# Kernel optimization log

Measured on AMD Instinct MI355X. Metric: run time of the kernel, lower is better.

## Reference

```python
import jax, jax.numpy as jnp
import numpy as np

EPS_BN = 1e-5
EPS_LN = 1e-5
EPS_L2 = 1e-12


def adder2d(x, w, stride):
    """AdderNet pseudo-conv: out = -sum |x_patch - w| (negative L1 distance).
    x: (N, Cin, H, W); w: (Cout, Cin, kh, kw); no padding, no bias.
    Loops only over the small fixed kernel footprint (<=12 positions) to avoid
    materializing the full im2col L1 tensor at once.
    """
    N, Cin, H, W = x.shape
    Cout, _, kh, kw = w.shape
    sh, sw = stride
    Ho = (H - kh) // sh + 1
    Wo = (W - kw) // sw + 1
    out = jnp.zeros((N, Ho, Wo, Cout), dtype=x.dtype)
    for i in range(kh):
        for j in range(kw):
            # strided slice of the input for this kernel tap: (N, Cin, Ho, Wo)
            xs = x[:, :, i:i + sh * Ho:sh, j:j + sw * Wo:sw]
            xs = jnp.transpose(xs, (0, 2, 3, 1))          # (N, Ho, Wo, Cin)
            wt = w[:, :, i, j]                            # (Cout, Cin)
            # |x - w| summed over Cin -> (N, Ho, Wo, Cout)
            out = out - jnp.abs(xs[:, :, :, None, :] - wt[None, None, None, :, :]).sum(-1)
    return jnp.transpose(out, (0, 3, 1, 2))               # (N, Cout, Ho, Wo)


def bn_relu(x, gamma, beta):
    # training-mode BatchNorm2d (batch statistics, biased var) + ReLU
    mean = x.mean(axis=(0, 2, 3), keepdims=True)
    var = x.var(axis=(0, 2, 3), keepdims=True)
    y = (x - mean) * jax.lax.rsqrt(var + EPS_BN)
    y = y * gamma[None, :, None, None] + beta[None, :, None, None]
    return jax.nn.relu(y)


def setup_inputs() -> dict:
    key = jax.random.key(0)
    ks = jax.random.split(key, 8)
    N = 16
    x = jax.random.normal(ks[0], (N, 1, 196, 3), dtype=jnp.float32)
    w1 = jax.random.normal(ks[1], (128, 1, 6, 1), dtype=jnp.float32) * 0.1
    w2 = jax.random.normal(ks[2], (256, 128, 6, 1), dtype=jnp.float32) * 0.05
    w3 = jax.random.normal(ks[3], (384, 256, 6, 2), dtype=jnp.float32) * 0.05
    g1, b1 = jnp.ones((128,), jnp.float32), jnp.zeros((128,), jnp.float32)
    g2, b2 = jnp.ones((256,), jnp.float32), jnp.zeros((256,), jnp.float32)
    g3, b3 = jnp.ones((384,), jnp.float32), jnp.zeros((384,), jnp.float32)
    Wfc = jax.random.normal(ks[4], (6, 16128), dtype=jnp.float32) * (1.0 / np.sqrt(16128))
    bfc = jax.random.normal(ks[5], (6,), dtype=jnp.float32) * 0.01
    return {"x": x, "w1": w1, "g1": g1, "b1": b1, "w2": w2, "g2": g2, "b2": b2,
            "w3": w3, "g3": g3, "b3": b3, "Wfc": Wfc, "bfc": bfc}


def reference(x, w1, g1, b1, w2, g2, b2, w3, g3, b3, Wfc, bfc):
    h = bn_relu(adder2d(x, w1, (2, 1)), g1, b1)   # (N,128,96,3)
    h = bn_relu(adder2d(h, w2, (2, 1)), g2, b2)   # (N,256,46,3)
    h = bn_relu(adder2d(h, w3, (2, 1)), g3, b3)   # (N,384,21,2)
    h = h.reshape(h.shape[0], -1)                  # (N,16128)
    h = h @ Wfc.T + bfc                            # (N,6)
    # nn.LayerNorm(x.size()) normalizes over ALL dims (batch included), weight=1 bias=0
    mu = h.mean()
    var = h.var()
    h = (h - mu) * jax.lax.rsqrt(var + EPS_LN)
    # F.normalize: per-row L2 normalization
    norm = jnp.sqrt((h * h).sum(axis=1, keepdims=True))
    return h / jnp.maximum(norm, EPS_L2)
```

## Files before the change

### kernel.cpp

```cpp
#include <hip/hip_runtime.h>
#include <math.h>

#define DEVINL __device__ __forceinline__

DEVINL float absadd(float a, float b) {
  float t;
  asm("v_add_f32 %0, |%1|, |%2|" : "=v"(t) : "v"(a), "v"(b));
  return t;
}

template<int NWAVES>
DEVINL void block_reduce_2d(double& a, double& b) {
  #pragma unroll
  for (int off = 32; off > 0; off >>= 1) {
    a += __shfl_down(a, off, 64);
    b += __shfl_down(b, off, 64);
  }
  __shared__ double sa[NWAVES], sb[NWAVES];
  const int tid = threadIdx.x;
  const int wid = tid >> 6;
  if ((tid & 63) == 0) { sa[wid] = a; sb[wid] = b; }
  __syncthreads();
  if (tid == 0) {
    double ta = 0.0, tb = 0.0;
    #pragma unroll
    for (int w = 0; w < NWAVES; ++w) { ta += sa[w]; tb += sb[w]; }
    a = ta; b = tb;
  }
}

__global__ __launch_bounds__(256) void k_conv1(
    const float* __restrict__ x, const float* __restrict__ w1,
    const float* __restrict__ g1, const float* __restrict__ b1,
    float* __restrict__ h1) {
  __shared__ float xlds[9408];
  const int co = blockIdx.x;
  const int tid = threadIdx.x;
  {
    float4* xd = (float4*)xlds;
    const float4* xs = (const float4*)x;
    #pragma unroll
    for (int k = 0; k < 10; ++k) {
      const int f = tid + k * 256;
      if (f < 2352) xd[f] = xs[f];
    }
  }
  float wv[6];
  #pragma unroll
  for (int i = 0; i < 6; ++i) wv[i] = w1[co * 6 + i];
  __syncthreads();

  float vals[18];
  double s = 0.0, sq = 0.0;
  #pragma unroll
  for (int k = 0; k < 18; ++k) {
    const int p = tid + k * 256;
    const int n = p / 288;
    const int r = p - n * 288;
    const int ho = r / 3;
    const int wo = r - ho * 3;
    const float* xb = xlds + n * 588 + (2 * ho) * 3 + wo;
    float e0 = xb[0]  - wv[0];
    float e1 = xb[3]  - wv[1];
    float e2 = xb[6]  - wv[2];
    float e3 = xb[9]  - wv[3];
    float e4 = xb[12] - wv[4];
    float e5 = xb[15] - wv[5];
    const float t0 = absadd(e0, e1);
    const float t1 = absadd(e2, e3);
    const float t2 = absadd(e4, e5);
    const float v = -((t0 + t1) + t2);
    vals[k] = v;
    s += (double)v;
    sq += (double)v * (double)v;
  }
  block_reduce_2d<4>(s, sq);
  __shared__ float ssc, ssh;
  if (tid == 0) {
    const double mean = s * (1.0 / 4608.0);
    const double var  = sq * (1.0 / 4608.0) - mean * mean;
    const float rstd = (float)rsqrt(var + 1e-5);
    const float sc = g1[co] * rstd;
    ssc = sc;
    ssh = b1[co] - (float)mean * sc;
  }
  __syncthreads();
  const float sc = ssc, sh = ssh;
  #pragma unroll
  for (int k = 0; k < 18; ++k) {
    const int p = tid + k * 256;
    const int n = p / 288;
    const int r = p - n * 288;
    const int ho = r / 3;
    const int wo = r - ho * 3;
    h1[((n * 128 + co) * 96 + ho) * 3 + wo] = fmaxf(0.f, fmaf(vals[k], sc, sh));
  }
}

__global__ __launch_bounds__(128) void k_conv2p(
    const float* __restrict__ h1, const float* __restrict__ w2,
    float* __restrict__ part2) {
  __shared__ float wlds[1024];
  __shared__ float2 xbuf[2][616];
  __shared__ float accbuf[64][71];
  const int bx = blockIdx.x;
  const int kc = bx & 7;
  const int rbx = bx >> 3;
  const int cg = rbx & 31;
  const int rbx2 = rbx >> 5;
  const int hoh = rbx2 & 1;
  const int nh = rbx2 >> 1;
  const int co0 = cg * 8, ci0 = kc * 16, n0 = nh * 8;
  const int tid = threadIdx.x;
  const int wvid = tid >> 6;
  const int lane = tid & 63;
  #pragma unroll
  for (int k = 0; k < 8; ++k) {
    const int f = wvid * 512 + lane + k * 64;
    const int cil = f >> 6, rem = f & 63, c = rem >> 3, kk = rem & 7;
    wlds[f] = (kk < 6) ? w2[(co0 + c) * 768 + (ci0 + cil) * 6 + kk] : 0.f;
  }
  const int n = lane >> 3, co = lane & 7;

  int s_lds[10], s_g[10];
  const bool v10 = lane < 24;
  #pragma unroll
  for (int k = 0; k < 10; ++k) {
    const int f = lane + k * 64;
    const int nn = f / 75, j = f - nn * 75;
    s_lds[k] = nn * 77 + j;
    s_g[k]   = (n0 + nn) * 18432 + 69 * hoh + j;
  }
  const float2* h1v = (const float2*)h1;
  const int cibase = ci0 + wvid * 8;

  float acc[69];
  #pragma unroll
  for (int i = 0; i < 69; ++i) acc[i] = 0.f;

  float2 r[10];
  #pragma unroll
  for (int k = 0; k < 9; ++k) r[k] = h1v[s_g[k] + cibase * 144];
  if (v10) r[9] = h1v[s_g[9] + cibase * 144];

  const float2* xrow2 = xbuf[wvid] + n * 77;
  const float4* wl4 = (const float4*)wlds;

  #pragma unroll 1
  for (int cil = 0; cil < 8; ++cil) {
    #pragma unroll
    for (int k = 0; k < 9; ++k) xbuf[wvid][s_lds[k]] = r[k];
    if (v10) xbuf[wvid][s_lds[9]] = r[9];
    if (cil + 1 < 8) {
      #pragma unroll
      for (int k = 0; k < 9; ++k) r[k] = h1v[s_g[k] + (cibase + cil + 1) * 144];
      if (v10) r[9] = h1v[s_g[9] + (cibase + cil + 1) * 144];
    }
    const int cl = wvid * 8 + cil;
    const float4 wa = wl4[(cl * 8 + co) * 2];
    const float4 wb = wl4[(cl * 8 + co) * 2 + 1];
    const float wv[6] = {wa.x, wa.y, wa.z, wa.w, wb.x, wb.y};
    float xf[18];
    #pragma unroll
    for (int t = 0; t < 9; ++t) {
      const float2 q = xrow2[t];
      xf[2 * t] = q.x; xf[2 * t + 1] = q.y;
    }
    #pragma unroll
    for (int h = 0; h < 23; ++h) {
      if (h > 0) {
        #pragma unroll
        for (int t = 0; t < 12; ++t) xf[t] = xf[t + 6];
        #pragma unroll
        for (int t = 0; t < 3; ++t) {
          const float2 q = xrow2[3 * h + 6 + t];
          xf[12 + 2 * t] = q.x; xf[13 + 2 * t] = q.y;
        }
      }
      #pragma unroll
      for (int wo = 0; wo < 3; ++wo) {
        float e0 = xf[0  + wo] - wv[0];
        float e1 = xf[3  + wo] - wv[1];
        float e2 = xf[6  + wo] - wv[2];
        float e3 = xf[9  + wo] - wv[3];
        float e4 = xf[12 + wo] - wv[4];
        float e5 = xf[15 + wo] - wv[5];
        const float t0 = absadd(e0, e1);
        const float t1 = absadd(e2, e3);
        const float t2 = absadd(e4, e5);
        acc[h * 3 + wo] += (t0 + t1) + t2;
      }
    }
  }
  if (wvid == 1) {
    #pragma unroll
    for (int i = 0; i < 69; ++i) accbuf[lane][i] = acc[i];
  }
  __syncthreads();
  if (wvid == 0) {
    #pragma unroll
    for (int i = 0; i < 69; ++i) acc[i] += accbuf[lane][i];
    float* dst = part2 + (size_t)(kc * 256 + co0 + co) * 2208 + (n0 + n) * 138 + 69 * hoh;
    #pragma unroll
    for (int i = 0; i < 69; ++i) dst[i] = acc[i];
  }
}

__global__ __launch_bounds__(384) void k_combine2(
    const float* __restrict__ part2, const float* __restrict__ g2,
    const float* __restrict__ b2, float* __restrict__ h2) {
  const int co = blockIdx.x;
  const int tid = threadIdx.x;
  const bool active = tid < 368;
  float v[6];
  double s = 0.0, sq = 0.0;
  #pragma unroll
  for (int k = 0; k < 6; ++k) {
    float sum = 0.f;
    if (active) {
      const int p = tid + k * 368;
      #pragma unroll
      for (int kc = 0; kc < 8; ++kc)
        sum += part2[(size_t)(kc * 256 + co) * 2208 + p];
    }
    const float val = -sum;
    v[k] = val;
    if (active) { s += (double)val; sq += (double)val * (double)val; }
  }
  block_reduce_2d<6>(s, sq);
  __shared__ float ssc, ssh;
  if (tid == 0) {
    const double mean = s * (1.0 / 2208.0);
    const double var  = sq * (1.0 / 2208.0) - mean * mean;
    const float rstd = (float)rsqrt(var + 1e-5);
    const float sc = g2[co] * rstd;
    ssc = sc;
    ssh = b2[co] - (float)mean * sc;
  }
  __syncthreads();
  if (active) {
    const float sc = ssc, sh = ssh;
    #pragma unroll
    for (int k = 0; k < 6; ++k) {
      const int p = tid + k * 368;
      const int n = p / 138, rem = p - n * 138;
      h2[n * 35328 + co * 138 + rem] = fmaxf(0.f, fmaf(v[k], sc, sh));
    }
  }
}

__global__ __launch_bounds__(128) void k_conv3p(
    const float* __restrict__ h2, const float* __restrict__ w3,
    float* __restrict__ part3) {
  __shared__ float wlds[1536];
  __shared__ float2 xbuf[2][560];
  __shared__ float accbuf[64][43];
  const int bx = blockIdx.x;
  const int kc = bx & 15;
  const int rbx = bx >> 4;
  const int cg = rbx % 48;
  const int nh = rbx / 48;
  const int co0 = cg * 8, ci0 = kc * 16, n0 = nh * 8;
  const int tid = threadIdx.x;
  const int wvid = tid >> 6;
  const int lane = tid & 63;
  #pragma unroll
  for (int k = 0; k < 12; ++k) {
    const int f = wvid * 768 + lane + k * 64;
    const int cil = f / 96, rem = f - cil * 96, c = rem / 12, kk = rem - c * 12;
    wlds[f] = w3[(co0 + c) * 3072 + (ci0 + cil) * 12 + kk];
  }
  const int n = lane >> 3, co = lane & 7;

  int s_lds[9], s_g[9];
  const bool v9 = lane < 40;
  #pragma unroll
  for (int k = 0; k < 9; ++k) {
    const int f = lane + k * 64;
    const int nn = f / 69, j = f - nn * 69;
    s_lds[k] = nn * 70 + j;
    s_g[k]   = (n0 + nn) * 17664 + j;
  }
  const float2* h2v = (const float2*)h2;
  const int cibase = ci0 + wvid * 8;

  float acc[42];
  #pragma unroll
  for (int i = 0; i < 42; ++i) acc[i] = 0.f;

  float2 r[9];
  #pragma unroll
  for (int k = 0; k < 8; ++k) r[k] = h2v[s_g[k] + cibase * 69];
  if (v9) r[8] = h2v[s_g[8] + cibase * 69];

  const float2* xrow2 = xbuf[wvid] + n * 70;
  const float4* wl4 = (const float4*)wlds;

  #pragma unroll 1
  for (int cil = 0; cil < 8; ++cil) {
    #pragma unroll
    for (int k = 0; k < 8; ++k) xbuf[wvid][s_lds[k]] = r[k];
    if (v9) xbuf[wvid][s_lds[8]] = r[8];
    if (cil + 1 < 8) {
      #pragma unroll
      for (int k = 0; k < 8; ++k) r[k] = h2v[s_g[k] + (cibase + cil + 1) * 69];
      if (v9) r[8] = h2v[s_g[8] + (cibase + cil + 1) * 69];
    }
    const int cl = wvid * 8 + cil;
    const float4 w0 = wl4[(cl * 8 + co) * 3];
    const float4 w1 = wl4[(cl * 8 + co) * 3 + 1];
    const float4 w2q = wl4[(cl * 8 + co) * 3 + 2];
    const float wv[12] = {w0.x, w0.y, w0.z, w0.w, w1.x, w1.y,
                          w1.z, w1.w, w2q.x, w2q.y, w2q.z, w2q.w};
    float xf[30];
    #pragma unroll
    for (int t = 0; t < 15; ++t) {
      const float2 q = xrow2[t];
      xf[2 * t + 0] = q.x; xf[2 * t + 1] = q.y;
    }
    #pragma unroll
    for (int hot = 0; hot < 7; ++hot) {
      #pragma unroll
      for (int h = 0; h < 3; ++h)
        #pragma unroll
        for (int wo = 0; wo < 2; ++wo) {
          float e0  = xf[(2 * h + 0) * 3 + wo]     - wv[0];
          float e1  = xf[(2 * h + 0) * 3 + wo + 1] - wv[1];
          float e2  = xf[(2 * h + 1) * 3 + wo]     - wv[2];
          float e3  = xf[(2 * h + 1) * 3 + wo + 1] - wv[3];
          float e4  = xf[(2 * h + 2) * 3 + wo]     - wv[4];
          float e5  = xf[(2 * h + 2) * 3 + wo + 1] - wv[5];
          float e6  = xf[(2 * h + 3) * 3 + wo]     - wv[6];
          float e7  = xf[(2 * h + 3) * 3 + wo + 1] - wv[7];
          float e8  = xf[(2 * h + 4) * 3 + wo]     - wv[8];
          float e9  = xf[(2 * h + 4) * 3 + wo + 1] - wv[9];
          float e10 = xf[(2 * h + 5) * 3 + wo]     - wv[10];
          float e11 = xf[(2 * h + 5) * 3 + wo + 1] - wv[11];
          const float t0 = absadd(e0, e1);
          const float t1 = absadd(e2, e3);
          const float t2 = absadd(e4, e5);
          const float t3 = absadd(e6, e7);
          const float t4 = absadd(e8, e9);
          const float t5 = absadd(e10, e11);
          acc[(3 * hot + h) * 2 + wo] += ((t0 + t1) + (t2 + t3)) + (t4 + t5);
        }
      if (hot < 6) {
        #pragma unroll
        for (int t = 0; t < 12; ++t) xf[t] = xf[t + 18];
        #pragma unroll
        for (int t = 0; t < 9; ++t) {
          const float2 q = xrow2[9 * hot + 15 + t];
          xf[12 + 2 * t] = q.x; xf[13 + 2 * t] = q.y;
        }
      }
    }
  }
  if (wvid == 1) {
    #pragma unroll
    for (int i = 0; i < 42; ++i) accbuf[lane][i] = acc[i];
  }
  __syncthreads();
  if (wvid == 0) {
    #pragma unroll
    for (int i = 0; i < 42; ++i) acc[i] += accbuf[lane][i];
    float2* dst = (float2*)(part3 + (size_t)(kc * 384 + co0 + co) * 672 + (n0 + n) * 42);
    #pragma unroll
    for (int k = 0; k < 21; ++k) dst[k] = make_float2(acc[2 * k], acc[2 * k + 1]);
  }
}

__global__ __launch_bounds__(384) void k_combine3(
    const float* __restrict__ part3, const float* __restrict__ g3,
    const float* __restrict__ b3, float* __restrict__ h3) {
  const int co = blockIdx.x;
  const int tid = threadIdx.x;
  const bool active = tid < 336;
  float v[2];
  double s = 0.0, sq = 0.0;
  #pragma unroll
  for (int k = 0; k < 2; ++k) {
    float sum = 0.f;
    if (active) {
      const int p = tid + k * 336;
      #pragma unroll
      for (int kc = 0; kc < 16; ++kc)
        sum += part3[(size_t)(kc * 384 + co) * 672 + p];
    }
    const float val = -sum;
    v[k] = val;
    if (active) { s += (double)val; sq += (double)val * (double)val; }
  }
  block_reduce_2d<6>(s, sq);
  __shared__ float ssc, ssh;
  if (tid == 0) {
    const double mean = s * (1.0 / 672.0);
    const double var  = sq * (1.0 / 672.0) - mean * mean;
    const float rstd = (float)rsqrt(var + 1e-5);
    const float sc = g3[co] * rstd;
    ssc = sc;
    ssh = b3[co] - (float)mean * sc;
  }
  __syncthreads();
  if (active) {
    const float sc = ssc, sh = ssh;
    #pragma unroll
    for (int k = 0; k < 2; ++k) {
      const int p = tid + k * 336;
      const int n = p / 42, rem = p - n * 42;
      h3[n * 16128 + co * 42 + rem] = fmaxf(0.f, fmaf(v[k], sc, sh));
    }
  }
}

__global__ __launch_bounds__(256) void k_fcp(
    const float* __restrict__ h3, const float* __restrict__ Wfc,
    float* __restrict__ hfcp) {
  const int bx = blockIdx.x;
  const int pair = bx >> 2, q = bx & 3;
  const int n = pair / 6, o = pair - n * 6;
  const float4* xr = (const float4*)(h3 + n * 16128) + q * 1008;
  const float4* wr = (const float4*)(Wfc + o * 16128) + q * 1008;
  float sacc = 0.f;
  for (int k = threadIdx.x; k < 1008; k += 256) {
    const float4 xv = xr[k];
    const float4 wv = wr[k];
    sacc += xv.x * wv.x + xv.y * wv.y + xv.z * wv.z + xv.w * wv.w;
  }
  double d = (double)sacc, dummy = 0.0;
  block_reduce_2d<4>(d, dummy);
  if (threadIdx.x == 0) hfcp[bx] = (float)d;
}

__global__ __launch_bounds__(128) void k_final(
    const float* __restrict__ hfcp, const float* __restrict__ bfc,
    float* __restrict__ out) {
  __shared__ float ys[96];
  __shared__ float params[2];
  const int tid = threadIdx.x;
  float v = 0.f;
  if (tid < 96) {
    v = hfcp[tid * 4 + 0] + hfcp[tid * 4 + 1] + hfcp[tid * 4 + 2] + hfcp[tid * 4 + 3]
        + bfc[tid % 6];
    ys[tid] = v;
  }
  __syncthreads();
  if (tid == 0) {
    double s = 0.0, sq = 0.0;
    for (int i = 0; i < 96; ++i) { const double t = (double)ys[i]; s += t; sq += t * t; }
    const double mu = s / 96.0;
    const double var = sq / 96.0 - mu * mu;
    params[0] = (float)mu;
    params[1] = (float)rsqrt(var + 1e-5);
  }
  __syncthreads();
  const float y = (v - params[0]) * params[1];
  __syncthreads();
  if (tid < 96) ys[tid] = y;
  __syncthreads();
  if (tid < 96) {
    const int n = tid / 6;
    float ss = 0.f;
    #pragma unroll
    for (int k = 0; k < 6; ++k) { const float t = ys[n * 6 + k]; ss += t * t; }
    const float norm = sqrtf(ss);
    out[tid] = y / fmaxf(norm, 1e-12f);
  }
}

extern "C" void kernel_launch(void* const* d_in, const int* in_sizes, int n_in,
                              void* d_out, int out_size, void* d_ws, size_t ws_size,
                              hipStream_t stream) {
  const float* x   = (const float*)d_in[0];
  const float* w1  = (const float*)d_in[1];
  const float* g1  = (const float*)d_in[2];
  const float* b1  = (const float*)d_in[3];
  const float* w2  = (const float*)d_in[4];
  const float* g2  = (const float*)d_in[5];
  const float* b2  = (const float*)d_in[6];
  const float* w3  = (const float*)d_in[7];
  const float* g3  = (const float*)d_in[8];
  const float* b3  = (const float*)d_in[9];
  const float* Wfc = (const float*)d_in[10];
  const float* bfc = (const float*)d_in[11];

  float* ws   = (float*)d_ws;
  float* h1   = ws;
  float* h2   = h1 + 589824;
  float* h3   = h2 + 565248;
  float* hfcp = h3 + 258048;
  float* part = hfcp + 384;
  float* out  = (float*)d_out;

  k_conv1   <<<128, 256, 0, stream>>>(x, w1, g1, b1, h1);
  k_conv2p  <<<1024, 128, 0, stream>>>(h1, w2, part);
  k_combine2<<<256, 384, 0, stream>>>(part, g2, b2, h2);
  k_conv3p  <<<1536, 128, 0, stream>>>(h2, w3, part);
  k_combine3<<<384, 384, 0, stream>>>(part, g3, b3, h3);
  k_fcp     <<<384, 256, 0, stream>>>(h3, Wfc, hfcp);
  k_final   <<<1, 128, 0, stream>>>(hfcp, bfc, out);
}
```

Baseline: 108.9 us.

## Split input-channel chunk across four waves per block in conv2/conv3 partial kernels

The two adder-conv partial kernels now launch 256 threads (four waves) per block instead of 128. Each wave handles 4 input channels instead of 8, which halves the serial per-wave loop and doubles the waves available to hide latency. The cross-wave reduction is rewritten as a chunked LDS reduction that reuses the input staging buffer. The cost is extra shared-memory reduction passes and barriers, plus more register pressure per block, which could limit occupancy given the large per-thread accumulator arrays.

```diff
diff --git a/kernel.cpp b/kernel.cpp
--- a/kernel.cpp
+++ b/kernel.cpp
@@ -97,12 +97,11 @@
   }
 }
 
-__global__ __launch_bounds__(128) void k_conv2p(
+__global__ __launch_bounds__(256) void k_conv2p(
     const float* __restrict__ h1, const float* __restrict__ w2,
     float* __restrict__ part2) {
   __shared__ float wlds[1024];
-  __shared__ float2 xbuf[2][616];
-  __shared__ float accbuf[64][71];
+  __shared__ float2 xbuf4[4][616];
   const int bx = blockIdx.x;
   const int kc = bx & 7;
   const int rbx = bx >> 3;
@@ -115,8 +114,8 @@
   const int wvid = tid >> 6;
   const int lane = tid & 63;
   #pragma unroll
-  for (int k = 0; k < 8; ++k) {
-    const int f = wvid * 512 + lane + k * 64;
+  for (int k = 0; k < 4; ++k) {
+    const int f = wvid * 256 + lane + k * 64;
     const int cil = f >> 6, rem = f & 63, c = rem >> 3, kk = rem & 7;
     wlds[f] = (kk < 6) ? w2[(co0 + c) * 768 + (ci0 + cil) * 6 + kk] : 0.f;
   }
@@ -132,7 +131,7 @@
     s_g[k]   = (n0 + nn) * 18432 + 69 * hoh + j;
   }
   const float2* h1v = (const float2*)h1;
-  const int cibase = ci0 + wvid * 8;
+  const int cibase = ci0 + wvid * 4;
 
   float acc[69];
   #pragma unroll
@@ -143,20 +142,20 @@
   for (int k = 0; k < 9; ++k) r[k] = h1v[s_g[k] + cibase * 144];
   if (v10) r[9] = h1v[s_g[9] + cibase * 144];
 
-  const float2* xrow2 = xbuf[wvid] + n * 77;
+  const float2* xrow2 = xbuf4[wvid] + n * 77;
   const float4* wl4 = (const float4*)wlds;
 
   #pragma unroll 1
-  for (int cil = 0; cil < 8; ++cil) {
-    #pragma unroll
-    for (int k = 0; k < 9; ++k) xbuf[wvid][s_lds[k]] = r[k];
-    if (v10) xbuf[wvid][s_lds[9]] = r[9];
-    if (cil + 1 < 8) {
+  for (int cil = 0; cil < 4; ++cil) {
+    #pragma unroll
+    for (int k = 0; k < 9; ++k) xbuf4[wvid][s_lds[k]] = r[k];
+    if (v10) xbuf4[wvid][s_lds[9]] = r[9];
+    if (cil + 1 < 4) {
       #pragma unroll
       for (int k = 0; k < 9; ++k) r[k] = h1v[s_g[k] + (cibase + cil + 1) * 144];
       if (v10) r[9] = h1v[s_g[9] + (cibase + cil + 1) * 144];
     }
-    const int cl = wvid * 8 + cil;
+    const int cl = wvid * 4 + cil;
     const float4 wa = wl4[(cl * 8 + co) * 2];
     const float4 wb = wl4[(cl * 8 + co) * 2 + 1];
     const float wv[6] = {wa.x, wa.y, wa.z, wa.w, wb.x, wb.y};
@@ -192,14 +191,26 @@
       }
     }
   }
-  if (wvid == 1) {
-    #pragma unroll
-    for (int i = 0; i < 69; ++i) accbuf[lane][i] = acc[i];
-  }
-  __syncthreads();
+  __syncthreads();
+  float* accb = (float*)xbuf4;
+  #pragma unroll 1
+  for (int chunk = 0; chunk < 3; ++chunk) {
+    if (wvid > 0) {
+      #pragma unroll
+      for (int i = 0; i < 23; ++i)
+        accb[((wvid - 1) * 64 + lane) * 24 + i] = acc[chunk * 23 + i];
+    }
+    __syncthreads();
+    if (wvid == 0) {
+      #pragma unroll
+      for (int w = 0; w < 3; ++w)
+        #pragma unroll
+        for (int i = 0; i < 23; ++i)
+          acc[chunk * 23 + i] += accb[(w * 64 + lane) * 24 + i];
+    }
+    __syncthreads();
+  }
   if (wvid == 0) {
-    #pragma unroll
-    for (int i = 0; i < 69; ++i) acc[i] += accbuf[lane][i];
     float* dst = part2 + (size_t)(kc * 256 + co0 + co) * 2208 + (n0 + n) * 138 + 69 * hoh;
     #pragma unroll
     for (int i = 0; i < 69; ++i) dst[i] = acc[i];
@@ -249,12 +260,11 @@
   }
 }
 
-__global__ __launch_bounds__(128) void k_conv3p(
+__global__ __launch_bounds__(256) void k_conv3p(
     const float* __restrict__ h2, const float* __restrict__ w3,
     float* __restrict__ part3) {
   __shared__ float wlds[1536];
-  __shared__ float2 xbuf[2][560];
-  __shared__ float accbuf[64][43];
+  __shared__ float2 xbuf4[4][560];
   const int bx = blockIdx.x;
   const int kc = bx & 15;
   const int rbx = bx >> 4;
@@ -265,8 +275,8 @@
   const int wvid = tid >> 6;
   const int lane = tid & 63;
   #pragma unroll
-  for (int k = 0; k < 12; ++k) {
-    const int f = wvid * 768 + lane + k * 64;
+  for (int k = 0; k < 6; ++k) {
+    const int f = wvid * 384 + lane + k * 64;
     const int cil = f / 96, rem = f - cil * 96, c = rem / 12, kk = rem - c * 12;
     wlds[f] = w3[(co0 + c) * 3072 + (ci0 + cil) * 12 + kk];
   }
@@ -282,7 +292,7 @@
     s_g[k]   = (n0 + nn) * 17664 + j;
   }
   const float2* h2v = (const float2*)h2;
-  const int cibase = ci0 + wvid * 8;
+  const int cibase = ci0 + wvid * 4;
 
   float acc[42];
   #pragma unroll
@@ -293,20 +303,20 @@
   for (int k = 0; k < 8; ++k) r[k] = h2v[s_g[k] + cibase * 69];
   if (v9) r[8] = h2v[s_g[8] + cibase * 69];
 
-  const float2* xrow2 = xbuf[wvid] + n * 70;
+  const float2* xrow2 = xbuf4[wvid] + n * 70;
   const float4* wl4 = (const float4*)wlds;
 
   #pragma unroll 1
-  for (int cil = 0; cil < 8; ++cil) {
-    #pragma unroll
-    for (int k = 0; k < 8; ++k) xbuf[wvid][s_lds[k]] = r[k];
-    if (v9) xbuf[wvid][s_lds[8]] = r[8];
-    if (cil + 1 < 8) {
+  for (int cil = 0; cil < 4; ++cil) {
+    #pragma unroll
+    for (int k = 0; k < 8; ++k) xbuf4[wvid][s_lds[k]] = r[k];
+    if (v9) xbuf4[wvid][s_lds[8]] = r[8];
+    if (cil + 1 < 4) {
       #pragma unroll
       for (int k = 0; k < 8; ++k) r[k] = h2v[s_g[k] + (cibase + cil + 1) * 69];
       if (v9) r[8] = h2v[s_g[8] + (cibase + cil + 1) * 69];
     }
-    const int cl = wvid * 8 + cil;
+    const int cl = wvid * 4 + cil;
     const float4 w0 = wl4[(cl * 8 + co) * 3];
     const float4 w1 = wl4[(cl * 8 + co) * 3 + 1];
     const float4 w2q = wl4[(cl * 8 + co) * 3 + 2];
@@ -355,14 +365,26 @@
       }
     }
   }
-  if (wvid == 1) {
-    #pragma unroll
-    for (int i = 0; i < 42; ++i) accbuf[lane][i] = acc[i];
-  }
-  __syncthreads();
+  __syncthreads();
+  float* accb = (float*)xbuf4;
+  #pragma unroll 1
+  for (int chunk = 0; chunk < 2; ++chunk) {
+    if (wvid > 0) {
+      #pragma unroll
+      for (int i = 0; i < 21; ++i)
+        accb[((wvid - 1) * 64 + lane) * 22 + i] = acc[chunk * 21 + i];
+    }
+    __syncthreads();
+    if (wvid == 0) {
+      #pragma unroll
+      for (int w = 0; w < 3; ++w)
+        #pragma unroll
+        for (int i = 0; i < 21; ++i)
+          acc[chunk * 21 + i] += accb[(w * 64 + lane) * 22 + i];
+    }
+    __syncthreads();
+  }
   if (wvid == 0) {
-    #pragma unroll
-    for (int i = 0; i < 42; ++i) acc[i] += accbuf[lane][i];
     float2* dst = (float2*)(part3 + (size_t)(kc * 384 + co0 + co) * 672 + (n0 + n) * 42);
     #pragma unroll
     for (int k = 0; k < 21; ++k) dst[k] = make_float2(acc[2 * k], acc[2 * k + 1]);
@@ -492,9 +514,9 @@
   float* out  = (float*)d_out;
 
   k_conv1   <<<128, 256, 0, stream>>>(x, w1, g1, b1, h1);
-  k_conv2p  <<<1024, 128, 0, stream>>>(h1, w2, part);
+  k_conv2p  <<<1024, 256, 0, stream>>>(h1, w2, part);
   k_combine2<<<256, 384, 0, stream>>>(part, g2, b2, h2);
-  k_conv3p  <<<1536, 128, 0, stream>>>(h2, w3, part);
+  k_conv3p  <<<1536, 256, 0, stream>>>(h2, w3, part);
   k_combine3<<<384, 384, 0, stream>>>(part, g3, b3, h3);
   k_fcp     <<<384, 256, 0, stream>>>(h3, Wfc, hfcp);
   k_final   <<<1, 128, 0, stream>>>(hfcp, bfc, out);
```

Result: slower. 143.5 us (+31.8%).
